# Kernel tuning notes

Hardware: AMD Instinct MI355X
Metric: run time of the kernel (lower is better)

Reference implementation:

```python
import jax, jax.numpy as jnp
import numpy as np
from jax import lax

D_MODEL = 1024
D_STATE = 16
D_CONV = 4
D_INNER = 2 * D_MODEL
BATCH = 2
SEQ = 1024


def setup_inputs() -> dict:
    key = jax.random.key(0)
    ks = jax.random.split(key, 8)
    std = 0.02
    return {
        "x": jax.random.normal(ks[0], (BATCH, SEQ, D_MODEL), jnp.float32),
        "in_proj_w": jax.random.normal(ks[1], (2 * D_INNER, D_MODEL), jnp.float32) * std,
        "conv_w": jax.random.normal(ks[2], (D_INNER, 1, D_CONV), jnp.float32) * 0.1,
        "x_proj_w": jax.random.normal(ks[3], (D_STATE + 1, D_INNER), jnp.float32) * std,
        "dt_w": jax.random.normal(ks[4], (D_INNER, 1), jnp.float32) * std,
        "dt_b": jnp.zeros((D_INNER,), jnp.float32),
        "A_param": jax.random.normal(ks[5], (D_INNER, D_STATE), jnp.float32) * std,
        "D_param": jnp.ones((D_INNER,), jnp.float32),
        "out_w": jax.random.normal(ks[6], (D_MODEL, D_INNER), jnp.float32) * std,
        "out_b": jnp.zeros((D_MODEL,), jnp.float32),
    }


def _silu(v):
    return v * jax.nn.sigmoid(v)


def _mamba_forward(x, in_proj_w, conv_w, x_proj_w, dt_w, dt_b, A_param, D_param, out_w, out_b):
    B, L, _ = x.shape
    # in_proj: [B,L,2*d_inner]
    xz = jnp.einsum('bld,ed->ble', x, in_proj_w)
    u, z = jnp.split(xz, 2, axis=-1)  # each [B,L,d_inner]
    # depthwise causal conv1d along time
    uc = u.transpose(0, 2, 1)  # [B,d_inner,L]
    uc = lax.conv_general_dilated(
        uc, conv_w, window_strides=(1,), padding=[(D_CONV - 1, D_CONV - 1)],
        dimension_numbers=('NCH', 'OIH', 'NCH'), feature_group_count=D_INNER,
    )[:, :, :L]
    u = _silu(uc.transpose(0, 2, 1))  # [B,L,d_inner]
    # x_proj -> (dt scalar, B coeffs)
    x_dbl = jnp.einsum('bld,ed->ble', u, x_proj_w)  # [B,L,d_state+1]
    dt_in = x_dbl[..., :1]                          # [B,L,1]
    Bmat = x_dbl[..., 1:]                           # [B,L,d_state]
    delta = jax.nn.softplus(dt_in * dt_w[:, 0] + dt_b)  # [B,L,d_inner]
    A = -jnp.exp(A_param)                            # [d_inner,d_state]

    # selective scan (time-major lax.scan)
    def step(h, inp):
        d_t, b_t = inp  # [B,d_inner], [B,d_state]
        h = jnp.exp(A * d_t[..., None]) * h + d_t[..., None] * b_t[:, None, :]
        y = jnp.einsum('bdn,bn->bd', h, b_t)
        return h, y

    h0 = jnp.zeros((B, D_INNER, D_STATE), x.dtype)
    _, ys = lax.scan(step, h0, (delta.transpose(1, 0, 2), Bmat.transpose(1, 0, 2)))
    y = ys.transpose(1, 0, 2) + u * D_param  # [B,L,d_inner]
    y = y * _silu(z)
    return jnp.einsum('bld,ed->ble', y, out_w) + out_b


def reference(x, in_proj_w, conv_w, x_proj_w, dt_w, dt_b, A_param, D_param, out_w, out_b):
    return _mamba_forward(x, in_proj_w, conv_w, x_proj_w, dt_w, dt_b, A_param, D_param, out_w, out_b)
```

## Files before the change

### kernel.cpp

```cpp
#include <hip/hip_runtime.h>
#include <stdint.h>
#include <stddef.h>

#define D_MODEL 1024
#define D_STATE 16
#define D_INNER 2048
#define BATCH   2
#define SEQ     1024
#define MROWS   (BATCH*SEQ)

#define NCH 32
#define TCH (SEQ/NCH)
#define NREC (BATCH*D_INNER*D_STATE)

#define XKS 8
#define XKC (D_INNER/XKS)

typedef __bf16 bf16x8 __attribute__((ext_vector_type(8)));
typedef float  f32x4  __attribute__((ext_vector_type(4)));
typedef unsigned short u16x8 __attribute__((ext_vector_type(8)));

__device__ __forceinline__ unsigned short f2bf(float f) {
    unsigned int u = __float_as_uint(f);
    u += 0x7fffu + ((u >> 16) & 1u);
    return (unsigned short)(u >> 16);
}
__device__ __forceinline__ float bf2f(unsigned short v) {
    return __uint_as_float((unsigned int)v << 16);
}

__device__ __forceinline__ void gl_lds16(const unsigned short* g, unsigned short* l) {
    __builtin_amdgcn_global_load_lds(
        (const __attribute__((address_space(1))) unsigned int*)g,
        (__attribute__((address_space(3))) unsigned int*)l, 16, 0, 0);
}

__global__ void cvt_all_kernel(const float* __restrict__ x,
                               const float* __restrict__ w1,
                               const float* __restrict__ w2,
                               const float* __restrict__ xw,
                               const float* __restrict__ ob,
                               const float* __restrict__ Ap,
                               unsigned short* __restrict__ xb,
                               unsigned short* __restrict__ wbi,
                               unsigned short* __restrict__ wbo,
                               unsigned short* __restrict__ wbp,
                               float* __restrict__ outp,
                               float* __restrict__ aAg,
                               float* __restrict__ dti,
                               float* __restrict__ Bm) {
    int blk = blockIdx.x, tid = threadIdx.x;
    if (blk < 8192) {
        const float* src; unsigned short* dst; int i;
        if (blk < 2048)      { src = x;  dst = xb;  i = blk * 1024 + tid * 4; }
        else if (blk < 6144) { src = w1; dst = wbi; i = (blk - 2048) * 1024 + tid * 4; }
        else                 { src = w2; dst = wbo; i = (blk - 6144) * 1024 + tid * 4; }
        float4 v = *(const float4*)(src + i);
        ushort4 o;
        o.x = f2bf(v.x); o.y = f2bf(v.y); o.z = f2bf(v.z); o.w = f2bf(v.w);
        *(ushort4*)(dst + i) = o;
    } else if (blk < 8448) {
        int id = (blk - 8192) * 256 + tid;
        wbp[id] = (id < 17 * D_INNER) ? f2bf(xw[id]) : (unsigned short)0;
    } else if (blk < 10496) {
        int i = (blk - 8448) * 1024 + tid * 4;
        int n = i & (D_MODEL - 1);
        *(float4*)(outp + i) = *(const float4*)(ob + n);
    } else if (blk < 10528) {
        int i = (blk - 10496) * 1024 + tid * 4;
        float4 a = *(const float4*)(Ap + i);
        float4 r;
        r.x = -__expf(a.x); r.y = -__expf(a.y);
        r.z = -__expf(a.z); r.w = -__expf(a.w);
        *(float4*)(aAg + i) = r;
    } else if (blk < 10530) {
        int i = (blk - 10528) * 1024 + tid * 4;
        *(float4*)(dti + i) = float4{0.f, 0.f, 0.f, 0.f};
    } else {
        int i = (blk - 10530) * 1024 + tid * 4;
        *(float4*)(Bm + i) = float4{0.f, 0.f, 0.f, 0.f};
    }
}

template<int NT, bool SPLITK2, bool OUT_BF16>
__global__ void gemm_bf16_kernel(const unsigned short* __restrict__ A,
                                 const unsigned short* __restrict__ Bw,
                                 void* __restrict__ Cv,
                                 int M, int N, int K) {
    constexpr int NTW = NT / 32;
    constexpr int BCH = NT / 8;
    constexpr int LPW = 4 + BCH / 4;
    __shared__ __align__(16) unsigned short Al[2][2 * 128 * 32];
    __shared__ __align__(16) unsigned short Bl[2][2 * NT * 32];

    const int tid  = threadIdx.x;
    const int lane = tid & 63;
    const int wid  = tid >> 6;
    const int wm   = wid >> 1;
    const int wn   = wid & 1;
    const int ln   = lane & 15;
    const int q    = lane >> 4;
    const int mblk = blockIdx.y * 128;
    const int nblk = blockIdx.x * NT;
    const int srow = lane >> 2;
    const int spart = lane & 3;

    const int kbeg = SPLITK2 ? blockIdx.z * (K / 2) : 0;
    const int kend = SPLITK2 ? kbeg + K / 2 : K;

    f32x4 acc[4][NTW] = {};

    auto stage = [&](int buf, int k0) {
        #pragma unroll
        for (int h = 0; h < 4; ++h) {
            int j = wid * 4 + h;
            int kh = j & 1, rb = j >> 1;
            int row = rb * 16 + srow;
            gl_lds16(A + (size_t)(mblk + row) * K + k0 + kh * 32 + spart * 8,
                     Al[buf] + kh * 4096 + rb * 512);
        }
        #pragma unroll
        for (int h = 0; h < BCH / 4; ++h) {
            int j = wid * (BCH / 4) + h;
            int kh = j & 1, rb = j >> 1;
            int row = rb * 16 + srow;
            gl_lds16(Bw + (size_t)(nblk + row) * K + k0 + kh * 32 + spart * 8,
                     Bl[buf] + kh * (NT * 32) + rb * 512);
        }
    };

    const int niter = (kend - kbeg) >> 6;
    stage(0, kbeg);
    int cur = 0;

    for (int it = 0; it < niter; ++it) {
        int k0 = kbeg + (it << 6);
        if (it + 1 < niter) {
            stage(cur ^ 1, k0 + 64);
            if constexpr (LPW == 8) asm volatile("s_waitcnt vmcnt(8)" ::: "memory");
            else                    asm volatile("s_waitcnt vmcnt(6)" ::: "memory");
        } else {
            asm volatile("s_waitcnt vmcnt(0)" ::: "memory");
        }
        __builtin_amdgcn_sched_barrier(0);
        __builtin_amdgcn_s_barrier();
        __builtin_amdgcn_sched_barrier(0);

        #pragma unroll
        for (int kh = 0; kh < 2; ++kh) {
            bf16x8 af[4], bfr[NTW];
            #pragma unroll
            for (int mt = 0; mt < 4; ++mt)
                af[mt] = *(const bf16x8*)(Al[cur] + kh * 4096 + (wm * 64 + mt * 16 + ln) * 32 + q * 8);
            #pragma unroll
            for (int nt = 0; nt < NTW; ++nt)
                bfr[nt] = *(const bf16x8*)(Bl[cur] + kh * (NT * 32) + (wn * (NT/2) + nt * 16 + ln) * 32 + q * 8);
            #pragma unroll
            for (int mt = 0; mt < 4; ++mt)
                #pragma unroll
                for (int nt = 0; nt < NTW; ++nt)
                    acc[mt][nt] = __builtin_amdgcn_mfma_f32_16x16x32_bf16(
                        af[mt], bfr[nt], acc[mt][nt], 0, 0, 0);
        }

        __builtin_amdgcn_sched_barrier(0);
        __builtin_amdgcn_s_barrier();
        cur ^= 1;
    }

    #pragma unroll
    for (int mt = 0; mt < 4; ++mt) {
        #pragma unroll
        for (int nt = 0; nt < NTW; ++nt) {
            int col = nblk + wn * (NT/2) + nt * 16 + ln;
            #pragma unroll
            for (int r = 0; r < 4; ++r) {
                int row = mblk + wm * 64 + mt * 16 + q * 4 + r;
                if (SPLITK2) {
                    atomicAdd((float*)Cv + (size_t)row * N + col, acc[mt][nt][r]);
                } else if (OUT_BF16) {
                    ((unsigned short*)Cv)[(size_t)row * N + col] = f2bf(acc[mt][nt][r]);
                } else {
                    ((float*)Cv)[(size_t)row * N + col] = acc[mt][nt][r];
                }
            }
        }
    }
}

__global__ void conv_silu_kernel(const unsigned short* __restrict__ xzb,
                                 const float* __restrict__ conv_w,
                                 unsigned short* __restrict__ ub) {
    int idx = blockIdx.x * 256 + threadIdx.x;
    int d8 = idx & 255;
    int m = idx >> 8;
    int l = m & (SEQ - 1);
    int d = d8 * 8;
    const float4* wv = (const float4*)(conv_w + (size_t)d * 4);
    float4 w[8];
    #pragma unroll
    for (int e = 0; e < 8; ++e) w[e] = wv[e];
    float s[8] = {0.f, 0.f, 0.f, 0.f, 0.f, 0.f, 0.f, 0.f};
    #pragma unroll
    for (int j = 0; j < 4; ++j) {
        if (l - j >= 0) {
            u16x8 r = *(const u16x8*)(xzb + (size_t)(m - j) * 4096 + d);
            #pragma unroll
            for (int e = 0; e < 8; ++e) {
                float wt = (j == 0) ? w[e].w : (j == 1) ? w[e].z
                         : (j == 2) ? w[e].y : w[e].x;
                s[e] += wt * bf2f(r[e]);
            }
        }
    }
    u16x8 o;
    #pragma unroll
    for (int e = 0; e < 8; ++e) {
        float sig = 1.f / (1.f + __expf(-s[e]));
        o[e] = f2bf(s[e] * sig);
    }
    *(u16x8*)(ub + (size_t)m * D_INNER + d) = o;
}

__global__ void xproj_mfma_kernel(const unsigned short* __restrict__ ub,
                                  const unsigned short* __restrict__ wbp,
                                  float* __restrict__ dti,
                                  float* __restrict__ Bm) {
    __shared__ __align__(16) unsigned short Al[2][64 * 64];
    __shared__ __align__(16) unsigned short Bl[2][32 * 64];

    const int tid  = threadIdx.x;
    const int lane = tid & 63;
    const int wid  = tid >> 6;
    const int ln   = lane & 15;
    const int q    = lane >> 4;
    const int m0   = blockIdx.y * 64;
    const int ks   = blockIdx.x;
    const int srow = lane >> 3;
    const int spart = lane & 7;

    f32x4 acc[2] = {};

    auto stage = [&](int buf, int it) {
        int k0 = ks * XKC + it * 64;
        #pragma unroll
        for (int h = 0; h < 2; ++h) {
            int j = wid * 2 + h;
            int row = j * 8 + srow;
            gl_lds16(ub + (size_t)(m0 + row) * D_INNER + k0 + spart * 8, Al[buf] + j * 512);
        }
        {
            int row = wid * 8 + srow;
            gl_lds16(wbp + (size_t)row * D_INNER + k0 + spart * 8, Bl[buf] + wid * 512);
        }
    };

    stage(0, 0);
    __syncthreads();
    int cur = 0;

    for (int it = 0; it < 4; ++it) {
        if (it < 3) stage(cur ^ 1, it + 1);

        bf16x8 af[2], bfr[2][2];
        #pragma unroll
        for (int kh = 0; kh < 2; ++kh) {
            af[kh] = *(const bf16x8*)(Al[cur] + (wid * 16 + ln) * 64 + kh * 32 + q * 8);
            bfr[0][kh] = *(const bf16x8*)(Bl[cur] + (0 * 16 + ln) * 64 + kh * 32 + q * 8);
            bfr[1][kh] = *(const bf16x8*)(Bl[cur] + (1 * 16 + ln) * 64 + kh * 32 + q * 8);
        }
        #pragma unroll
        for (int kh = 0; kh < 2; ++kh) {
            acc[0] = __builtin_amdgcn_mfma_f32_16x16x32_bf16(af[kh], bfr[0][kh], acc[0], 0, 0, 0);
            acc[1] = __builtin_amdgcn_mfma_f32_16x16x32_bf16(af[kh], bfr[1][kh], acc[1], 0, 0, 0);
        }
        __syncthreads();
        cur ^= 1;
    }

    #pragma unroll
    for (int nf = 0; nf < 2; ++nf) {
        int col = nf * 16 + ln;
        #pragma unroll
        for (int r = 0; r < 4; ++r) {
            int m = m0 + wid * 16 + q * 4 + r;
            if (col == 0)       atomicAdd(dti + m, acc[nf][r]);
            else if (col < 17)  atomicAdd(Bm + (size_t)m * D_STATE + (col - 1), acc[nf][r]);
        }
    }
}

__device__ __forceinline__ float softplus_f(float xv) {
    return fmaxf(xv, 0.f) + __logf(1.f + __expf(-fabsf(xv)));
}

__global__ void scanA_kernel(const float* __restrict__ dt_in,
                             const float* __restrict__ Bm,
                             const float* __restrict__ dt_w,
                             const float* __restrict__ dt_b,
                             const float* __restrict__ aAg,
                             float* __restrict__ Pg,
                             float* __restrict__ Sg) {
    __shared__ float sdt[TCH];
    __shared__ float sB[TCH * D_STATE];
    const int tid = threadIdx.x;
    const int b = blockIdx.z, c = blockIdx.y;
    const int d = blockIdx.x * 256 + tid;

    if (tid < TCH) sdt[tid] = dt_in[b * SEQ + c * TCH + tid];
    if (tid < TCH * D_STATE / 4)
        ((float4*)sB)[tid] = ((const float4*)(Bm + ((size_t)(b * SEQ + c * TCH)) * D_STATE))[tid];
    __syncthreads();

    const float dtw = dt_w[d], dtb = dt_b[d];
    float aA[D_STATE], h[D_STATE];
    #pragma unroll
    for (int n4 = 0; n4 < 4; ++n4) {
        float4 av = ((const float4*)(aAg + (size_t)d * D_STATE))[n4];
        aA[n4*4+0] = av.x; aA[n4*4+1] = av.y;
        aA[n4*4+2] = av.z; aA[n4*4+3] = av.w;
    }
    #pragma unroll
    for (int n = 0; n < D_STATE; ++n) h[n] = 0.f;
    float tsum = 0.f;

    for (int t = 0; t < TCH; ++t) {
        float sp = softplus_f(sdt[t] * dtw + dtb);
        tsum += sp;
        #pragma unroll
        for (int n = 0; n < D_STATE; ++n) {
            float a = __expf(aA[n] * sp);
            h[n] = a * h[n] + sp * sB[t * D_STATE + n];
        }
    }

    size_t base = (size_t)c * NREC + ((size_t)(b * D_INNER + d)) * D_STATE;
    #pragma unroll
    for (int n4 = 0; n4 < 4; ++n4) {
        float4 pv, sv;
        pv.x = __expf(aA[n4*4+0] * tsum); pv.y = __expf(aA[n4*4+1] * tsum);
        pv.z = __expf(aA[n4*4+2] * tsum); pv.w = __expf(aA[n4*4+3] * tsum);
        sv.x = h[n4*4+0]; sv.y = h[n4*4+1]; sv.z = h[n4*4+2]; sv.w = h[n4*4+3];
        *(float4*)(Pg + base + n4 * 4) = pv;
        *(float4*)(Sg + base + n4 * 4) = sv;
    }
}

__global__ void scanB_kernel(const float* __restrict__ Pg,
                             const float* __restrict__ Sg,
                             float* __restrict__ Hin) {
    int idx = blockIdx.x * 256 + threadIdx.x;
    float h = 0.f;
    #pragma unroll
    for (int c = 0; c < NCH; ++c) {
        size_t o = (size_t)c * NREC + idx;
        Hin[o] = h;
        h = Pg[o] * h + Sg[o];
    }
}

__global__ void scanC_kernel(const float* __restrict__ dt_in,
                             const float* __restrict__ Bm,
                             const float* __restrict__ dt_w,
                             const float* __restrict__ dt_b,
                             const float* __restrict__ aAg,
                             const float* __restrict__ Hin,
                             const unsigned short* __restrict__ ub,
                             const unsigned short* __restrict__ xzb,
                             const float* __restrict__ Dp,
                             unsigned short* __restrict__ ypb) {
    __shared__ float sdt[TCH];
    __shared__ float sB[TCH * D_STATE];
    const int tid = threadIdx.x;
    const int b = blockIdx.z, c = blockIdx.y;
    const int d = blockIdx.x * 256 + tid;

    if (tid < TCH) sdt[tid] = dt_in[b * SEQ + c * TCH + tid];
    if (tid < TCH * D_STATE / 4)
        ((float4*)sB)[tid] = ((const float4*)(Bm + ((size_t)(b * SEQ + c * TCH)) * D_STATE))[tid];
    __syncthreads();

    const float dtw = dt_w[d], dtb = dt_b[d];
    const float Dv = Dp[d];
    float aA[D_STATE], h[D_STATE];
    #pragma unroll
    for (int n4 = 0; n4 < 4; ++n4) {
        float4 av = ((const float4*)(aAg + (size_t)d * D_STATE))[n4];
        aA[n4*4+0] = av.x; aA[n4*4+1] = av.y;
        aA[n4*4+2] = av.z; aA[n4*4+3] = av.w;
    }
    size_t hbase = (size_t)c * NREC + ((size_t)(b * D_INNER + d)) * D_STATE;
    #pragma unroll
    for (int n4 = 0; n4 < 4; ++n4) {
        float4 hv = *(const float4*)(Hin + hbase + n4 * 4);
        h[n4*4+0] = hv.x; h[n4*4+1] = hv.y; h[n4*4+2] = hv.z; h[n4*4+3] = hv.w;
    }

    const size_t mrow0 = (size_t)b * SEQ + c * TCH;
    for (int t = 0; t < TCH; ++t) {
        float sp = softplus_f(sdt[t] * dtw + dtb);
        float y0 = 0.f, y1 = 0.f, y2 = 0.f, y3 = 0.f;
        #pragma unroll
        for (int n4 = 0; n4 < 4; ++n4) {
            #pragma unroll
            for (int j = 0; j < 4; ++j) {
                int n = n4 * 4 + j;
                float Bv = sB[t * D_STATE + n];
                float a = __expf(aA[n] * sp);
                h[n] = a * h[n] + sp * Bv;
                float p = h[n] * Bv;
                if (n4 == 0) y0 += p; else if (n4 == 1) y1 += p;
                else if (n4 == 2) y2 += p; else y3 += p;
            }
        }
        float y = (y0 + y1) + (y2 + y3);
        size_t m = mrow0 + t;
        float z  = bf2f(xzb[m * 4096 + D_INNER + d]);
        float sz = z / (1.f + __expf(-z));
        float uv = bf2f(ub[m * D_INNER + d]);
        ypb[m * D_INNER + d] = f2bf((y + uv * Dv) * sz);
    }
}

extern "C" void kernel_launch(void* const* d_in, const int* in_sizes, int n_in,
                              void* d_out, int out_size, void* d_ws, size_t ws_size,
                              hipStream_t stream) {
    const float* x         = (const float*)d_in[0];
    const float* in_proj_w = (const float*)d_in[1];
    const float* conv_w    = (const float*)d_in[2];
    const float* x_proj_w  = (const float*)d_in[3];
    const float* dt_w      = (const float*)d_in[4];
    const float* dt_b      = (const float*)d_in[5];
    const float* A_param   = (const float*)d_in[6];
    const float* D_param   = (const float*)d_in[7];
    const float* out_w     = (const float*)d_in[8];
    const float* out_b     = (const float*)d_in[9];
    float* out = (float*)d_out;

    char* ws = (char*)d_ws;
    unsigned short* xb  = (unsigned short*)(ws);
    unsigned short* wbi = (unsigned short*)(ws + (4u  << 20));
    unsigned short* wbo = (unsigned short*)(ws + (12u << 20));
    unsigned short* xzb = (unsigned short*)(ws + (16u << 20));
    unsigned short* ub  = (unsigned short*)(ws + (32u << 20));
    float*          dti = (float*)(ws + (40u << 20));
    float*          Bm  = (float*)(ws + (40u << 20) + (64u  << 10));
    unsigned short* wbp = (unsigned short*)(ws + (40u << 20) + (192u << 10));
    float*          aAg = (float*)(ws + (40u << 20) + (320u << 10));
    float*          Pg  = (float*)(ws + (44u << 20));
    float*          Sg  = (float*)(ws + (52u << 20));
    float*          Hin = (float*)(ws + (60u << 20));
    unsigned short* ypb = (unsigned short*)(ws + (68u << 20));

    cvt_all_kernel<<<dim3(10562), 256, 0, stream>>>(
        x, in_proj_w, out_w, x_proj_w, out_b, A_param,
        xb, wbi, wbo, wbp, out, aAg, dti, Bm);

    gemm_bf16_kernel<128, false, true><<<dim3(4096 / 128, MROWS / 128), 256, 0, stream>>>(
        xb, wbi, xzb, MROWS, 2 * D_INNER, D_MODEL);

    conv_silu_kernel<<<dim3(MROWS), 256, 0, stream>>>(xzb, conv_w, ub);

    xproj_mfma_kernel<<<dim3(XKS, MROWS / 64), 256, 0, stream>>>(ub, wbp, dti, Bm);

    scanA_kernel<<<dim3(D_INNER / 256, NCH, BATCH), 256, 0, stream>>>(
        dti, Bm, dt_w, dt_b, aAg, Pg, Sg);
    scanB_kernel<<<dim3(NREC / 256), 256, 0, stream>>>(Pg, Sg, Hin);
    scanC_kernel<<<dim3(D_INNER / 256, NCH, BATCH), 256, 0, stream>>>(
        dti, Bm, dt_w, dt_b, aAg, Hin, ub, xzb, D_param, ypb);

    gemm_bf16_kernel<64, true, false><<<dim3(1024 / 64, MROWS / 128, 2), 256, 0, stream>>>(
        ypb, wbo, out, MROWS, D_MODEL, D_INNER);
}
```

Before: 226.1 us.

## Fuse all pipeline stages into one cooperative persistent kernel with grid syncs

Replaces the eight separate kernel launches with a single cooperative mega-kernel of 512 blocks. Each stage (conversion, in_proj GEMM, conv+SiLU, x_proj, three scan phases, out_proj GEMM) runs as a block-strided section separated by grid.sync(). The aim is to remove per-launch overhead and inter-kernel gaps. In exchange, every stage is forced onto a fixed 512-block grid with 64KB of shared memory per block, which may lower occupancy and load balance. The x_proj split-K factor also rises from 8 to 16 so that stage covers the 512 blocks.

```diff
diff --git a/kernel.cpp b/kernel.cpp
--- a/kernel.cpp
+++ b/kernel.cpp
@@ -1,6 +1,9 @@
 #include <hip/hip_runtime.h>
+#include <hip/hip_cooperative_groups.h>
 #include <stdint.h>
 #include <stddef.h>
+
+namespace cg = cooperative_groups;
 
 #define D_MODEL 1024
 #define D_STATE 16
@@ -13,8 +16,12 @@
 #define TCH (SEQ/NCH)
 #define NREC (BATCH*D_INNER*D_STATE)
 
-#define XKS 8
+#define XKS 16
 #define XKC (D_INNER/XKS)
+
+#define NBLK 512
+#define NTHR 256
+#define NALL (NBLK*NTHR)
 
 typedef __bf16 bf16x8 __attribute__((ext_vector_type(8)));
 typedef float  f32x4  __attribute__((ext_vector_type(4)));
@@ -35,63 +42,29 @@
         (__attribute__((address_space(3))) unsigned int*)l, 16, 0, 0);
 }
 
-__global__ void cvt_all_kernel(const float* __restrict__ x,
-                               const float* __restrict__ w1,
-                               const float* __restrict__ w2,
-                               const float* __restrict__ xw,
-                               const float* __restrict__ ob,
-                               const float* __restrict__ Ap,
-                               unsigned short* __restrict__ xb,
-                               unsigned short* __restrict__ wbi,
-                               unsigned short* __restrict__ wbo,
-                               unsigned short* __restrict__ wbp,
-                               float* __restrict__ outp,
-                               float* __restrict__ aAg,
-                               float* __restrict__ dti,
-                               float* __restrict__ Bm) {
-    int blk = blockIdx.x, tid = threadIdx.x;
-    if (blk < 8192) {
-        const float* src; unsigned short* dst; int i;
-        if (blk < 2048)      { src = x;  dst = xb;  i = blk * 1024 + tid * 4; }
-        else if (blk < 6144) { src = w1; dst = wbi; i = (blk - 2048) * 1024 + tid * 4; }
-        else                 { src = w2; dst = wbo; i = (blk - 6144) * 1024 + tid * 4; }
-        float4 v = *(const float4*)(src + i);
-        ushort4 o;
-        o.x = f2bf(v.x); o.y = f2bf(v.y); o.z = f2bf(v.z); o.w = f2bf(v.w);
-        *(ushort4*)(dst + i) = o;
-    } else if (blk < 8448) {
-        int id = (blk - 8192) * 256 + tid;
-        wbp[id] = (id < 17 * D_INNER) ? f2bf(xw[id]) : (unsigned short)0;
-    } else if (blk < 10496) {
-        int i = (blk - 8448) * 1024 + tid * 4;
-        int n = i & (D_MODEL - 1);
-        *(float4*)(outp + i) = *(const float4*)(ob + n);
-    } else if (blk < 10528) {
-        int i = (blk - 10496) * 1024 + tid * 4;
-        float4 a = *(const float4*)(Ap + i);
-        float4 r;
-        r.x = -__expf(a.x); r.y = -__expf(a.y);
-        r.z = -__expf(a.z); r.w = -__expf(a.w);
-        *(float4*)(aAg + i) = r;
-    } else if (blk < 10530) {
-        int i = (blk - 10528) * 1024 + tid * 4;
-        *(float4*)(dti + i) = float4{0.f, 0.f, 0.f, 0.f};
-    } else {
-        int i = (blk - 10530) * 1024 + tid * 4;
-        *(float4*)(Bm + i) = float4{0.f, 0.f, 0.f, 0.f};
-    }
-}
-
-template<int NT, bool SPLITK2, bool OUT_BF16>
-__global__ void gemm_bf16_kernel(const unsigned short* __restrict__ A,
-                                 const unsigned short* __restrict__ Bw,
-                                 void* __restrict__ Cv,
-                                 int M, int N, int K) {
+__device__ __forceinline__ float softplus_f(float xv) {
+    return fmaxf(xv, 0.f) + __logf(1.f + __expf(-fabsf(xv)));
+}
+
+struct Params {
+    const float *x, *in_proj_w, *conv_w, *x_proj_w, *dt_w, *dt_b, *A_param, *D_param, *out_w, *out_b;
+    float* out;
+    unsigned short *xb, *wbi, *wbo, *xzb, *ub, *wbp, *ypb;
+    float *dti, *Bm, *aAg, *Pg, *Sg, *Hin;
+};
+
+template<int NT, bool ATOMIC, bool OUT_BF16>
+__device__ __forceinline__ void gemm_body(const unsigned short* __restrict__ A,
+                                          const unsigned short* __restrict__ Bw,
+                                          void* __restrict__ Cv,
+                                          int M, int N, int K,
+                                          char* smem, int bx, int by,
+                                          int kbeg, int kend) {
     constexpr int NTW = NT / 32;
     constexpr int BCH = NT / 8;
     constexpr int LPW = 4 + BCH / 4;
-    __shared__ __align__(16) unsigned short Al[2][2 * 128 * 32];
-    __shared__ __align__(16) unsigned short Bl[2][2 * NT * 32];
+    unsigned short* Als = (unsigned short*)smem;
+    unsigned short* Bls = (unsigned short*)(smem + 32768);
 
     const int tid  = threadIdx.x;
     const int lane = tid & 63;
@@ -100,24 +73,23 @@
     const int wn   = wid & 1;
     const int ln   = lane & 15;
     const int q    = lane >> 4;
-    const int mblk = blockIdx.y * 128;
-    const int nblk = blockIdx.x * NT;
+    const int mblk = by * 128;
+    const int nblk = bx * NT;
     const int srow = lane >> 2;
     const int spart = lane & 3;
 
-    const int kbeg = SPLITK2 ? blockIdx.z * (K / 2) : 0;
-    const int kend = SPLITK2 ? kbeg + K / 2 : K;
-
     f32x4 acc[4][NTW] = {};
 
     auto stage = [&](int buf, int k0) {
+        unsigned short* Ab = Als + buf * 8192;
+        unsigned short* Bb = Bls + buf * (2 * NT * 32);
         #pragma unroll
         for (int h = 0; h < 4; ++h) {
             int j = wid * 4 + h;
             int kh = j & 1, rb = j >> 1;
             int row = rb * 16 + srow;
             gl_lds16(A + (size_t)(mblk + row) * K + k0 + kh * 32 + spart * 8,
-                     Al[buf] + kh * 4096 + rb * 512);
+                     Ab + kh * 4096 + rb * 512);
         }
         #pragma unroll
         for (int h = 0; h < BCH / 4; ++h) {
@@ -125,7 +97,7 @@
             int kh = j & 1, rb = j >> 1;
             int row = rb * 16 + srow;
             gl_lds16(Bw + (size_t)(nblk + row) * K + k0 + kh * 32 + spart * 8,
-                     Bl[buf] + kh * (NT * 32) + rb * 512);
+                     Bb + kh * (NT * 32) + rb * 512);
         }
     };
 
@@ -151,10 +123,10 @@
             bf16x8 af[4], bfr[NTW];
             #pragma unroll
             for (int mt = 0; mt < 4; ++mt)
-                af[mt] = *(const bf16x8*)(Al[cur] + kh * 4096 + (wm * 64 + mt * 16 + ln) * 32 + q * 8);
+                af[mt] = *(const bf16x8*)(Als + cur * 8192 + kh * 4096 + (wm * 64 + mt * 16 + ln) * 32 + q * 8);
             #pragma unroll
             for (int nt = 0; nt < NTW; ++nt)
-                bfr[nt] = *(const bf16x8*)(Bl[cur] + kh * (NT * 32) + (wn * (NT/2) + nt * 16 + ln) * 32 + q * 8);
+                bfr[nt] = *(const bf16x8*)(Bls + cur * (2 * NT * 32) + kh * (NT * 32) + (wn * (NT/2) + nt * 16 + ln) * 32 + q * 8);
             #pragma unroll
             for (int mt = 0; mt < 4; ++mt)
                 #pragma unroll
@@ -176,299 +148,321 @@
             #pragma unroll
             for (int r = 0; r < 4; ++r) {
                 int row = mblk + wm * 64 + mt * 16 + q * 4 + r;
-                if (SPLITK2) {
+                if (ATOMIC)
                     atomicAdd((float*)Cv + (size_t)row * N + col, acc[mt][nt][r]);
-                } else if (OUT_BF16) {
+                else if (OUT_BF16)
                     ((unsigned short*)Cv)[(size_t)row * N + col] = f2bf(acc[mt][nt][r]);
-                } else {
+                else
                     ((float*)Cv)[(size_t)row * N + col] = acc[mt][nt][r];
+            }
+        }
+    }
+}
+
+__global__ __launch_bounds__(256, 2) void mega_kernel(Params p) {
+    __shared__ __align__(16) char smem[65536];
+    cg::grid_group grid = cg::this_grid();
+    const int tid = threadIdx.x;
+    const int bid = blockIdx.x;
+    const int gtid = bid * NTHR + tid;
+
+    {
+        for (int i = gtid * 4; i < 2097152; i += NALL * 4) {
+            float4 v = *(const float4*)(p.x + i);
+            ushort4 o; o.x = f2bf(v.x); o.y = f2bf(v.y); o.z = f2bf(v.z); o.w = f2bf(v.w);
+            *(ushort4*)(p.xb + i) = o;
+        }
+        for (int i = gtid * 4; i < 4194304; i += NALL * 4) {
+            float4 v = *(const float4*)(p.in_proj_w + i);
+            ushort4 o; o.x = f2bf(v.x); o.y = f2bf(v.y); o.z = f2bf(v.z); o.w = f2bf(v.w);
+            *(ushort4*)(p.wbi + i) = o;
+        }
+        for (int i = gtid * 4; i < 2097152; i += NALL * 4) {
+            float4 v = *(const float4*)(p.out_w + i);
+            ushort4 o; o.x = f2bf(v.x); o.y = f2bf(v.y); o.z = f2bf(v.z); o.w = f2bf(v.w);
+            *(ushort4*)(p.wbo + i) = o;
+        }
+        for (int i = gtid * 4; i < 2097152; i += NALL * 4) {
+            int n = i & (D_MODEL - 1);
+            *(float4*)(p.out + i) = *(const float4*)(p.out_b + n);
+        }
+        if (gtid < 8192) {
+            int i = gtid * 4;
+            float4 a = *(const float4*)(p.A_param + i);
+            float4 r;
+            r.x = -__expf(a.x); r.y = -__expf(a.y);
+            r.z = -__expf(a.z); r.w = -__expf(a.w);
+            *(float4*)(p.aAg + i) = r;
+        }
+        if (gtid < 8192) {
+            u16x8 o;
+            #pragma unroll
+            for (int e = 0; e < 8; ++e) {
+                int id = gtid * 8 + e;
+                o[e] = (id < 17 * D_INNER) ? f2bf(p.x_proj_w[id]) : (unsigned short)0;
+            }
+            *(u16x8*)(p.wbp + gtid * 8) = o;
+        }
+        if (gtid < 512)  *(float4*)(p.dti + gtid * 4) = float4{0.f, 0.f, 0.f, 0.f};
+        if (gtid < 8192) *(float4*)(p.Bm  + gtid * 4) = float4{0.f, 0.f, 0.f, 0.f};
+    }
+    grid.sync();
+
+    gemm_body<128, false, true>(p.xb, p.wbi, p.xzb, MROWS, 4096, 1024,
+                                smem, bid & 31, bid >> 5, 0, 1024);
+    grid.sync();
+
+    {
+        #pragma unroll
+        for (int r4 = 0; r4 < 4; ++r4) {
+            int m = bid * 4 + r4;
+            int l = m & (SEQ - 1);
+            int d = tid * 8;
+            const float4* wv = (const float4*)(p.conv_w + (size_t)d * 4);
+            float4 w[8];
+            #pragma unroll
+            for (int e = 0; e < 8; ++e) w[e] = wv[e];
+            float s[8] = {0.f, 0.f, 0.f, 0.f, 0.f, 0.f, 0.f, 0.f};
+            #pragma unroll
+            for (int j = 0; j < 4; ++j) {
+                if (l - j >= 0) {
+                    u16x8 rv = *(const u16x8*)(p.xzb + (size_t)(m - j) * 4096 + d);
+                    #pragma unroll
+                    for (int e = 0; e < 8; ++e) {
+                        float wt = (j == 0) ? w[e].w : (j == 1) ? w[e].z
+                                 : (j == 2) ? w[e].y : w[e].x;
+                        s[e] += wt * bf2f(rv[e]);
+                    }
                 }
             }
-        }
-    }
-}
-
-__global__ void conv_silu_kernel(const unsigned short* __restrict__ xzb,
-                                 const float* __restrict__ conv_w,
-                                 unsigned short* __restrict__ ub) {
-    int idx = blockIdx.x * 256 + threadIdx.x;
-    int d8 = idx & 255;
-    int m = idx >> 8;
-    int l = m & (SEQ - 1);
-    int d = d8 * 8;
-    const float4* wv = (const float4*)(conv_w + (size_t)d * 4);
-    float4 w[8];
-    #pragma unroll
-    for (int e = 0; e < 8; ++e) w[e] = wv[e];
-    float s[8] = {0.f, 0.f, 0.f, 0.f, 0.f, 0.f, 0.f, 0.f};
-    #pragma unroll
-    for (int j = 0; j < 4; ++j) {
-        if (l - j >= 0) {
-            u16x8 r = *(const u16x8*)(xzb + (size_t)(m - j) * 4096 + d);
+            u16x8 o;
             #pragma unroll
             for (int e = 0; e < 8; ++e) {
-                float wt = (j == 0) ? w[e].w : (j == 1) ? w[e].z
-                         : (j == 2) ? w[e].y : w[e].x;
-                s[e] += wt * bf2f(r[e]);
-            }
-        }
-    }
-    u16x8 o;
-    #pragma unroll
-    for (int e = 0; e < 8; ++e) {
-        float sig = 1.f / (1.f + __expf(-s[e]));
-        o[e] = f2bf(s[e] * sig);
-    }
-    *(u16x8*)(ub + (size_t)m * D_INNER + d) = o;
-}
-
-__global__ void xproj_mfma_kernel(const unsigned short* __restrict__ ub,
-                                  const unsigned short* __restrict__ wbp,
-                                  float* __restrict__ dti,
-                                  float* __restrict__ Bm) {
-    __shared__ __align__(16) unsigned short Al[2][64 * 64];
-    __shared__ __align__(16) unsigned short Bl[2][32 * 64];
-
-    const int tid  = threadIdx.x;
-    const int lane = tid & 63;
-    const int wid  = tid >> 6;
-    const int ln   = lane & 15;
-    const int q    = lane >> 4;
-    const int m0   = blockIdx.y * 64;
-    const int ks   = blockIdx.x;
-    const int srow = lane >> 3;
-    const int spart = lane & 7;
-
-    f32x4 acc[2] = {};
-
-    auto stage = [&](int buf, int it) {
-        int k0 = ks * XKC + it * 64;
-        #pragma unroll
-        for (int h = 0; h < 2; ++h) {
-            int j = wid * 2 + h;
-            int row = j * 8 + srow;
-            gl_lds16(ub + (size_t)(m0 + row) * D_INNER + k0 + spart * 8, Al[buf] + j * 512);
-        }
-        {
-            int row = wid * 8 + srow;
-            gl_lds16(wbp + (size_t)row * D_INNER + k0 + spart * 8, Bl[buf] + wid * 512);
-        }
-    };
-
-    stage(0, 0);
-    __syncthreads();
-    int cur = 0;
-
-    for (int it = 0; it < 4; ++it) {
-        if (it < 3) stage(cur ^ 1, it + 1);
-
-        bf16x8 af[2], bfr[2][2];
-        #pragma unroll
-        for (int kh = 0; kh < 2; ++kh) {
-            af[kh] = *(const bf16x8*)(Al[cur] + (wid * 16 + ln) * 64 + kh * 32 + q * 8);
-            bfr[0][kh] = *(const bf16x8*)(Bl[cur] + (0 * 16 + ln) * 64 + kh * 32 + q * 8);
-            bfr[1][kh] = *(const bf16x8*)(Bl[cur] + (1 * 16 + ln) * 64 + kh * 32 + q * 8);
-        }
-        #pragma unroll
-        for (int kh = 0; kh < 2; ++kh) {
-            acc[0] = __builtin_amdgcn_mfma_f32_16x16x32_bf16(af[kh], bfr[0][kh], acc[0], 0, 0, 0);
-            acc[1] = __builtin_amdgcn_mfma_f32_16x16x32_bf16(af[kh], bfr[1][kh], acc[1], 0, 0, 0);
-        }
+                float sig = 1.f / (1.f + __expf(-s[e]));
+                o[e] = f2bf(s[e] * sig);
+            }
+            *(u16x8*)(p.ub + (size_t)m * D_INNER + d) = o;
+        }
+    }
+    grid.sync();
+
+    {
+        unsigned short* Als = (unsigned short*)smem;
+        unsigned short* Bls = (unsigned short*)(smem + 16384);
+        const int lane = tid & 63;
+        const int wid  = tid >> 6;
+        const int ln   = lane & 15;
+        const int q    = lane >> 4;
+        const int ks   = bid & 15;
+        const int m0   = (bid >> 4) * 64;
+        const int srow = lane >> 3;
+        const int spart = lane & 7;
+
+        f32x4 acc[2] = {};
+
+        auto stage = [&](int buf, int it) {
+            int k0 = ks * XKC + it * 64;
+            unsigned short* Ab = Als + buf * 4096;
+            unsigned short* Bb = Bls + buf * 2048;
+            #pragma unroll
+            for (int h = 0; h < 2; ++h) {
+                int j = wid * 2 + h;
+                int row = j * 8 + srow;
+                gl_lds16(p.ub + (size_t)(m0 + row) * D_INNER + k0 + spart * 8, Ab + j * 512);
+            }
+            {
+                int row = wid * 8 + srow;
+                gl_lds16(p.wbp + (size_t)row * D_INNER + k0 + spart * 8, Bb + wid * 512);
+            }
+        };
+
+        stage(0, 0);
         __syncthreads();
-        cur ^= 1;
-    }
-
-    #pragma unroll
-    for (int nf = 0; nf < 2; ++nf) {
-        int col = nf * 16 + ln;
-        #pragma unroll
-        for (int r = 0; r < 4; ++r) {
-            int m = m0 + wid * 16 + q * 4 + r;
-            if (col == 0)       atomicAdd(dti + m, acc[nf][r]);
-            else if (col < 17)  atomicAdd(Bm + (size_t)m * D_STATE + (col - 1), acc[nf][r]);
-        }
-    }
-}
-
-__device__ __forceinline__ float softplus_f(float xv) {
-    return fmaxf(xv, 0.f) + __logf(1.f + __expf(-fabsf(xv)));
-}
-
-__global__ void scanA_kernel(const float* __restrict__ dt_in,
-                             const float* __restrict__ Bm,
-                             const float* __restrict__ dt_w,
-                             const float* __restrict__ dt_b,
-                             const float* __restrict__ aAg,
-                             float* __restrict__ Pg,
-                             float* __restrict__ Sg) {
-    __shared__ float sdt[TCH];
-    __shared__ float sB[TCH * D_STATE];
-    const int tid = threadIdx.x;
-    const int b = blockIdx.z, c = blockIdx.y;
-    const int d = blockIdx.x * 256 + tid;
-
-    if (tid < TCH) sdt[tid] = dt_in[b * SEQ + c * TCH + tid];
-    if (tid < TCH * D_STATE / 4)
-        ((float4*)sB)[tid] = ((const float4*)(Bm + ((size_t)(b * SEQ + c * TCH)) * D_STATE))[tid];
-    __syncthreads();
-
-    const float dtw = dt_w[d], dtb = dt_b[d];
-    float aA[D_STATE], h[D_STATE];
-    #pragma unroll
-    for (int n4 = 0; n4 < 4; ++n4) {
-        float4 av = ((const float4*)(aAg + (size_t)d * D_STATE))[n4];
-        aA[n4*4+0] = av.x; aA[n4*4+1] = av.y;
-        aA[n4*4+2] = av.z; aA[n4*4+3] = av.w;
-    }
-    #pragma unroll
-    for (int n = 0; n < D_STATE; ++n) h[n] = 0.f;
-    float tsum = 0.f;
-
-    for (int t = 0; t < TCH; ++t) {
-        float sp = softplus_f(sdt[t] * dtw + dtb);
-        tsum += sp;
-        #pragma unroll
-        for (int n = 0; n < D_STATE; ++n) {
-            float a = __expf(aA[n] * sp);
-            h[n] = a * h[n] + sp * sB[t * D_STATE + n];
-        }
-    }
-
-    size_t base = (size_t)c * NREC + ((size_t)(b * D_INNER + d)) * D_STATE;
-    #pragma unroll
-    for (int n4 = 0; n4 < 4; ++n4) {
-        float4 pv, sv;
-        pv.x = __expf(aA[n4*4+0] * tsum); pv.y = __expf(aA[n4*4+1] * tsum);
-        pv.z = __expf(aA[n4*4+2] * tsum); pv.w = __expf(aA[n4*4+3] * tsum);
-        sv.x = h[n4*4+0]; sv.y = h[n4*4+1]; sv.z = h[n4*4+2]; sv.w = h[n4*4+3];
-        *(float4*)(Pg + base + n4 * 4) = pv;
-        *(float4*)(Sg + base + n4 * 4) = sv;
-    }
-}
-
-__global__ void scanB_kernel(const float* __restrict__ Pg,
-                             const float* __restrict__ Sg,
-                             float* __restrict__ Hin) {
-    int idx = blockIdx.x * 256 + threadIdx.x;
-    float h = 0.f;
-    #pragma unroll
-    for (int c = 0; c < NCH; ++c) {
-        size_t o = (size_t)c * NREC + idx;
-        Hin[o] = h;
-        h = Pg[o] * h + Sg[o];
-    }
-}
-
-__global__ void scanC_kernel(const float* __restrict__ dt_in,
-                             const float* __restrict__ Bm,
-                             const float* __restrict__ dt_w,
-                             const float* __restrict__ dt_b,
-                             const float* __restrict__ aAg,
-                             const float* __restrict__ Hin,
-                             const unsigned short* __restrict__ ub,
-                             const unsigned short* __restrict__ xzb,
-                             const float* __restrict__ Dp,
-                             unsigned short* __restrict__ ypb) {
-    __shared__ float sdt[TCH];
-    __shared__ float sB[TCH * D_STATE];
-    const int tid = threadIdx.x;
-    const int b = blockIdx.z, c = blockIdx.y;
-    const int d = blockIdx.x * 256 + tid;
-
-    if (tid < TCH) sdt[tid] = dt_in[b * SEQ + c * TCH + tid];
-    if (tid < TCH * D_STATE / 4)
-        ((float4*)sB)[tid] = ((const float4*)(Bm + ((size_t)(b * SEQ + c * TCH)) * D_STATE))[tid];
-    __syncthreads();
-
-    const float dtw = dt_w[d], dtb = dt_b[d];
-    const float Dv = Dp[d];
-    float aA[D_STATE], h[D_STATE];
-    #pragma unroll
-    for (int n4 = 0; n4 < 4; ++n4) {
-        float4 av = ((const float4*)(aAg + (size_t)d * D_STATE))[n4];
-        aA[n4*4+0] = av.x; aA[n4*4+1] = av.y;
-        aA[n4*4+2] = av.z; aA[n4*4+3] = av.w;
-    }
-    size_t hbase = (size_t)c * NREC + ((size_t)(b * D_INNER + d)) * D_STATE;
-    #pragma unroll
-    for (int n4 = 0; n4 < 4; ++n4) {
-        float4 hv = *(const float4*)(Hin + hbase + n4 * 4);
-        h[n4*4+0] = hv.x; h[n4*4+1] = hv.y; h[n4*4+2] = hv.z; h[n4*4+3] = hv.w;
-    }
-
-    const size_t mrow0 = (size_t)b * SEQ + c * TCH;
-    for (int t = 0; t < TCH; ++t) {
-        float sp = softplus_f(sdt[t] * dtw + dtb);
-        float y0 = 0.f, y1 = 0.f, y2 = 0.f, y3 = 0.f;
+        int cur = 0;
+
+        for (int it = 0; it < 2; ++it) {
+            if (it < 1) stage(cur ^ 1, it + 1);
+
+            bf16x8 af[2], bfr[2][2];
+            #pragma unroll
+            for (int kh = 0; kh < 2; ++kh) {
+                af[kh] = *(const bf16x8*)(Als + cur * 4096 + (wid * 16 + ln) * 64 + kh * 32 + q * 8);
+                bfr[0][kh] = *(const bf16x8*)(Bls + cur * 2048 + (0 * 16 + ln) * 64 + kh * 32 + q * 8);
+                bfr[1][kh] = *(const bf16x8*)(Bls + cur * 2048 + (1 * 16 + ln) * 64 + kh * 32 + q * 8);
+            }
+            #pragma unroll
+            for (int kh = 0; kh < 2; ++kh) {
+                acc[0] = __builtin_amdgcn_mfma_f32_16x16x32_bf16(af[kh], bfr[0][kh], acc[0], 0, 0, 0);
+                acc[1] = __builtin_amdgcn_mfma_f32_16x16x32_bf16(af[kh], bfr[1][kh], acc[1], 0, 0, 0);
+            }
+            __syncthreads();
+            cur ^= 1;
+        }
+
+        #pragma unroll
+        for (int nf = 0; nf < 2; ++nf) {
+            int col = nf * 16 + ln;
+            #pragma unroll
+            for (int r = 0; r < 4; ++r) {
+                int m = m0 + wid * 16 + q * 4 + r;
+                if (col == 0)       atomicAdd(p.dti + m, acc[nf][r]);
+                else if (col < 17)  atomicAdd(p.Bm + (size_t)m * D_STATE + (col - 1), acc[nf][r]);
+            }
+        }
+    }
+    grid.sync();
+
+    {
+        float* sdt = (float*)smem;
+        float* sB  = (float*)(smem + 128);
+        const int dblk = bid & 7, c = (bid >> 3) & 31, b = bid >> 8;
+        const int d = dblk * 256 + tid;
+
+        if (tid < TCH) sdt[tid] = p.dti[b * SEQ + c * TCH + tid];
+        if (tid < TCH * D_STATE / 4)
+            ((float4*)sB)[tid] = ((const float4*)(p.Bm + ((size_t)(b * SEQ + c * TCH)) * D_STATE))[tid];
+        __syncthreads();
+
+        const float dtw = p.dt_w[d], dtb = p.dt_b[d];
+        float aA[D_STATE], h[D_STATE];
         #pragma unroll
         for (int n4 = 0; n4 < 4; ++n4) {
-            #pragma unroll
-            for (int j = 0; j < 4; ++j) {
-                int n = n4 * 4 + j;
-                float Bv = sB[t * D_STATE + n];
+            float4 av = ((const float4*)(p.aAg + (size_t)d * D_STATE))[n4];
+            aA[n4*4+0] = av.x; aA[n4*4+1] = av.y;
+            aA[n4*4+2] = av.z; aA[n4*4+3] = av.w;
+        }
+        #pragma unroll
+        for (int n = 0; n < D_STATE; ++n) h[n] = 0.f;
+        float tsum = 0.f;
+
+        for (int t = 0; t < TCH; ++t) {
+            float sp = softplus_f(sdt[t] * dtw + dtb);
+            tsum += sp;
+            #pragma unroll
+            for (int n = 0; n < D_STATE; ++n) {
                 float a = __expf(aA[n] * sp);
-                h[n] = a * h[n] + sp * Bv;
-                float p = h[n] * Bv;
-                if (n4 == 0) y0 += p; else if (n4 == 1) y1 += p;
-                else if (n4 == 2) y2 += p; else y3 += p;
-            }
-        }
-        float y = (y0 + y1) + (y2 + y3);
-        size_t m = mrow0 + t;
-        float z  = bf2f(xzb[m * 4096 + D_INNER + d]);
-        float sz = z / (1.f + __expf(-z));
-        float uv = bf2f(ub[m * D_INNER + d]);
-        ypb[m * D_INNER + d] = f2bf((y + uv * Dv) * sz);
-    }
+                h[n] = a * h[n] + sp * sB[t * D_STATE + n];
+            }
+        }
+
+        size_t base = (size_t)c * NREC + ((size_t)(b * D_INNER + d)) * D_STATE;
+        #pragma unroll
+        for (int n4 = 0; n4 < 4; ++n4) {
+            float4 pv, sv;
+            pv.x = __expf(aA[n4*4+0] * tsum); pv.y = __expf(aA[n4*4+1] * tsum);
+            pv.z = __expf(aA[n4*4+2] * tsum); pv.w = __expf(aA[n4*4+3] * tsum);
+            sv.x = h[n4*4+0]; sv.y = h[n4*4+1]; sv.z = h[n4*4+2]; sv.w = h[n4*4+3];
+            *(float4*)(p.Pg + base + n4 * 4) = pv;
+            *(float4*)(p.Sg + base + n4 * 4) = sv;
+        }
+        __syncthreads();
+    }
+    grid.sync();
+
+    if (bid < 256) {
+        int idx = bid * 256 + tid;
+        float h = 0.f;
+        #pragma unroll
+        for (int c = 0; c < NCH; ++c) {
+            size_t o = (size_t)c * NREC + idx;
+            p.Hin[o] = h;
+            h = p.Pg[o] * h + p.Sg[o];
+        }
+    }
+    grid.sync();
+
+    {
+        float* sdt = (float*)smem;
+        float* sB  = (float*)(smem + 128);
+        const int dblk = bid & 7, c = (bid >> 3) & 31, b = bid >> 8;
+        const int d = dblk * 256 + tid;
+
+        if (tid < TCH) sdt[tid] = p.dti[b * SEQ + c * TCH + tid];
+        if (tid < TCH * D_STATE / 4)
+            ((float4*)sB)[tid] = ((const float4*)(p.Bm + ((size_t)(b * SEQ + c * TCH)) * D_STATE))[tid];
+        __syncthreads();
+
+        const float dtw = p.dt_w[d], dtb = p.dt_b[d];
+        const float Dv = p.D_param[d];
+        float aA[D_STATE], h[D_STATE];
+        #pragma unroll
+        for (int n4 = 0; n4 < 4; ++n4) {
+            float4 av = ((const float4*)(p.aAg + (size_t)d * D_STATE))[n4];
+            aA[n4*4+0] = av.x; aA[n4*4+1] = av.y;
+            aA[n4*4+2] = av.z; aA[n4*4+3] = av.w;
+        }
+        size_t hbase = (size_t)c * NREC + ((size_t)(b * D_INNER + d)) * D_STATE;
+        #pragma unroll
+        for (int n4 = 0; n4 < 4; ++n4) {
+            float4 hv = *(const float4*)(p.Hin + hbase + n4 * 4);
+            h[n4*4+0] = hv.x; h[n4*4+1] = hv.y; h[n4*4+2] = hv.z; h[n4*4+3] = hv.w;
+        }
+
+        const size_t mrow0 = (size_t)b * SEQ + c * TCH;
+        for (int t = 0; t < TCH; ++t) {
+            float sp = softplus_f(sdt[t] * dtw + dtb);
+            float y0 = 0.f, y1 = 0.f, y2 = 0.f, y3 = 0.f;
+            #pragma unroll
+            for (int n4 = 0; n4 < 4; ++n4) {
+                #pragma unroll
+                for (int j = 0; j < 4; ++j) {
+                    int n = n4 * 4 + j;
+                    float Bv = sB[t * D_STATE + n];
+                    float a = __expf(aA[n] * sp);
+                    h[n] = a * h[n] + sp * Bv;
+                    float pmul = h[n] * Bv;
+                    if (n4 == 0) y0 += pmul; else if (n4 == 1) y1 += pmul;
+                    else if (n4 == 2) y2 += pmul; else y3 += pmul;
+                }
+            }
+            float y = (y0 + y1) + (y2 + y3);
+            size_t m = mrow0 + t;
+            float z  = bf2f(p.xzb[m * 4096 + D_INNER + d]);
+            float sz = z / (1.f + __expf(-z));
+            float uv = bf2f(p.ub[m * D_INNER + d]);
+            p.ypb[m * D_INNER + d] = f2bf((y + uv * Dv) * sz);
+        }
+        __syncthreads();
+    }
+    grid.sync();
+
+    gemm_body<64, true, false>(p.ypb, p.wbo, p.out, MROWS, 1024, 2048,
+                               smem, bid & 15, (bid >> 4) & 15,
+                               (bid >> 8) * 1024, (bid >> 8) * 1024 + 1024);
 }
 
 extern "C" void kernel_launch(void* const* d_in, const int* in_sizes, int n_in,
                               void* d_out, int out_size, void* d_ws, size_t ws_size,
                               hipStream_t stream) {
-    const float* x         = (const float*)d_in[0];
-    const float* in_proj_w = (const float*)d_in[1];
-    const float* conv_w    = (const float*)d_in[2];
-    const float* x_proj_w  = (const float*)d_in[3];
-    const float* dt_w      = (const float*)d_in[4];
-    const float* dt_b      = (const float*)d_in[5];
-    const float* A_param   = (const float*)d_in[6];
-    const float* D_param   = (const float*)d_in[7];
-    const float* out_w     = (const float*)d_in[8];
-    const float* out_b     = (const float*)d_in[9];
-    float* out = (float*)d_out;
-
     char* ws = (char*)d_ws;
-    unsigned short* xb  = (unsigned short*)(ws);
-    unsigned short* wbi = (unsigned short*)(ws + (4u  << 20));
-    unsigned short* wbo = (unsigned short*)(ws + (12u << 20));
-    unsigned short* xzb = (unsigned short*)(ws + (16u << 20));
-    unsigned short* ub  = (unsigned short*)(ws + (32u << 20));
-    float*          dti = (float*)(ws + (40u << 20));
-    float*          Bm  = (float*)(ws + (40u << 20) + (64u  << 10));
-    unsigned short* wbp = (unsigned short*)(ws + (40u << 20) + (192u << 10));
-    float*          aAg = (float*)(ws + (40u << 20) + (320u << 10));
-    float*          Pg  = (float*)(ws + (44u << 20));
-    float*          Sg  = (float*)(ws + (52u << 20));
-    float*          Hin = (float*)(ws + (60u << 20));
-    unsigned short* ypb = (unsigned short*)(ws + (68u << 20));
-
-    cvt_all_kernel<<<dim3(10562), 256, 0, stream>>>(
-        x, in_proj_w, out_w, x_proj_w, out_b, A_param,
-        xb, wbi, wbo, wbp, out, aAg, dti, Bm);
-
-    gemm_bf16_kernel<128, false, true><<<dim3(4096 / 128, MROWS / 128), 256, 0, stream>>>(
-        xb, wbi, xzb, MROWS, 2 * D_INNER, D_MODEL);
-
-    conv_silu_kernel<<<dim3(MROWS), 256, 0, stream>>>(xzb, conv_w, ub);
-
-    xproj_mfma_kernel<<<dim3(XKS, MROWS / 64), 256, 0, stream>>>(ub, wbp, dti, Bm);
-
-    scanA_kernel<<<dim3(D_INNER / 256, NCH, BATCH), 256, 0, stream>>>(
-        dti, Bm, dt_w, dt_b, aAg, Pg, Sg);
-    scanB_kernel<<<dim3(NREC / 256), 256, 0, stream>>>(Pg, Sg, Hin);
-    scanC_kernel<<<dim3(D_INNER / 256, NCH, BATCH), 256, 0, stream>>>(
-        dti, Bm, dt_w, dt_b, aAg, Hin, ub, xzb, D_param, ypb);
-
-    gemm_bf16_kernel<64, true, false><<<dim3(1024 / 64, MROWS / 128, 2), 256, 0, stream>>>(
-        ypb, wbo, out, MROWS, D_MODEL, D_INNER);
-}
+    Params p;
+    p.x         = (const float*)d_in[0];
+    p.in_proj_w = (const float*)d_in[1];
+    p.conv_w    = (const float*)d_in[2];
+    p.x_proj_w  = (const float*)d_in[3];
+    p.dt_w      = (const float*)d_in[4];
+    p.dt_b      = (const float*)d_in[5];
+    p.A_param   = (const float*)d_in[6];
+    p.D_param   = (const float*)d_in[7];
+    p.out_w     = (const float*)d_in[8];
+    p.out_b     = (const float*)d_in[9];
+    p.out = (float*)d_out;
+
+    p.xb  = (unsigned short*)(ws);
+    p.wbi = (unsigned short*)(ws + (4u  << 20));
+    p.wbo = (unsigned short*)(ws + (12u << 20));
+    p.xzb = (unsigned short*)(ws + (16u << 20));
+    p.ub  = (unsigned short*)(ws + (32u << 20));
+    p.dti = (float*)(ws + (40u << 20));
+    p.Bm  = (float*)(ws + (40u << 20) + (64u  << 10));
+    p.wbp = (unsigned short*)(ws + (40u << 20) + (192u << 10));
+    p.aAg = (float*)(ws + (40u << 20) + (320u << 10));
+    p.Pg  = (float*)(ws + (44u << 20));
+    p.Sg  = (float*)(ws + (52u << 20));
+    p.Hin = (float*)(ws + (60u << 20));
+    p.ypb = (unsigned short*)(ws + (68u << 20));
+
+    void* args[] = { (void*)&p };
+    hipLaunchCooperativeKernel((const void*)mega_kernel,
+                               dim3(NBLK), dim3(NTHR), args, 0, stream);
+}
```

Measured after the change: 648.2 us. 2.87x slower.
